# Kernel tuning notes

Hardware: AMD Instinct MI355X
Metric: run time of the kernel (lower is better)

## Reference

```python
import jax, jax.numpy as jnp
import numpy as np

DAMP_MIN = jnp.asarray([0.001, 0.001], dtype=jnp.float32)
B = 4194304


def setup_inputs() -> dict:
    key = jax.random.key(0)
    ks = jax.random.split(key, 14)
    rn = lambda k, s: jax.random.normal(k, s, dtype=jnp.float32)
    return {
        "x": rn(ks[0], (B, 2)),
        "w_d1": rn(ks[1], (2, 16)),
        "w_d2": rn(ks[2], (16, 16)),
        "w_d3": rn(ks[3], (16, 2)),
        "w_o1": rn(ks[4], (2, 16)),
        "w_o2": rn(ks[5], (16, 16)),
        "w_o3": rn(ks[6], (16, 1)),
        "b_d1": rn(ks[7], (16,)),
        "b_d2": rn(ks[8], (16,)),
        "b_d3": rn(ks[9], (2,)),
        "b_o1": rn(ks[10], (16,)),
        "b_o2": rn(ks[11], (16,)),
        "b_o3": rn(ks[12], (1,)),
    }


def reference(x, w_d1, w_d2, w_d3, w_o1, w_o2, w_o3,
              b_d1, b_d2, b_d3, b_o1, b_o2, b_o3) -> jnp.ndarray:
    # diag branch: 3-layer tanh MLP -> relu -> +damp_min -> * x   [B, 2]
    d = jnp.tanh(x @ w_d1 + b_d1)
    d = jnp.tanh(d @ w_d2 + b_d2)
    d3 = d @ w_d3 + b_d3
    d3r = (jax.nn.relu(d3) + DAMP_MIN) * x  # diag elements of L

    # off-diag branch: 3-layer tanh MLP -> scalar per sample   [B, 1]
    o = jnp.tanh(x @ w_o1 + b_o1)
    o = jnp.tanh(o @ w_o2 + b_o2)
    o3 = o @ w_o3 + b_o3

    # L = [[a, 0], [c, b]];  D_i = (L L^T) x_i, closed form for 2x2:
    # L L^T = [[a^2, a*c], [a*c, c^2 + b^2]]
    a = d3r[:, 0]
    b = d3r[:, 1]
    c = o3[:, 0]
    x0 = x[:, 0]
    x1 = x[:, 1]
    D0 = a * a * x0 + a * c * x1
    D1 = a * c * x0 + (c * c + b * b) * x1
    return jnp.stack([D0, D1], axis=1)  # [B, 2]
```

## Files before the change

### kernel.cpp

```cpp
#include <hip/hip_runtime.h>

#define BTOT 4194304
#define MPW 4

typedef __attribute__((ext_vector_type(4))) float f32x4;
typedef __attribute__((ext_vector_type(8))) short bf16x8;

__device__ __forceinline__ short f2bf(float f) {
  union { float f; unsigned u; } v; v.f = f;
  unsigned u = v.u;
  unsigned r = (u + 0x7FFFu + ((u >> 16) & 1u)) >> 16;
  return (short)r;
}
__device__ __forceinline__ float bf2f(short s) {
  union { unsigned u; float f; } v; v.u = ((unsigned)(unsigned short)s) << 16;
  return v.f;
}
__device__ __forceinline__ float tanh_fast(float x) {
  float t = __builtin_amdgcn_exp2f(x * 2.88539008177792681472f);
  float r = __builtin_amdgcn_rcpf(1.0f + t);
  return __builtin_fmaf(-2.0f, r, 1.0f);
}

__global__ __launch_bounds__(256, 4)
void damping_kernel(const float* __restrict__ x,
                    const float* __restrict__ w_d1, const float* __restrict__ w_d2,
                    const float* __restrict__ w_d3, const float* __restrict__ w_o1,
                    const float* __restrict__ w_o2, const float* __restrict__ w_o3,
                    const float* __restrict__ b_d1, const float* __restrict__ b_d2,
                    const float* __restrict__ b_d3, const float* __restrict__ b_o1,
                    const float* __restrict__ b_o2, const float* __restrict__ b_o3,
                    float* __restrict__ out)
{
  const int tid  = blockIdx.x * blockDim.x + threadIdx.x;
  const int wave = tid >> 6;
  const int l    = threadIdx.x & 63;
  const int g    = l >> 4;
  const int c16  = l & 15;
  const int kbase = g * 8;

  float W0[8], W1[8], B1[8];
  #pragma unroll
  for (int j = 0; j < 8; ++j) {
    int f = kbase + j;
    if (f < 16) { W0[j] = w_d1[f];      W1[j] = w_d1[16 + f];      B1[j] = b_d1[f]; }
    else        { W0[j] = w_o1[f - 16]; W1[j] = w_o1[16 + f - 16]; B1[j] = b_o1[f - 16]; }
  }
  bf16x8 Adh, Adl, Aoh, Aol;
  #pragma unroll
  for (int j = 0; j < 8; ++j) {
    int k = kbase + j;
    float ad = (k < 16)  ? w_d2[k * 16 + c16]        : 0.0f;
    float ao = (k >= 16) ? w_o2[(k - 16) * 16 + c16] : 0.0f;
    short adh = f2bf(ad); Adh[j] = adh; Adl[j] = f2bf(ad - bf2f(adh));
    short aoh = f2bf(ao); Aoh[j] = aoh; Aol[j] = f2bf(ao - bf2f(aoh));
  }
  f32x4 Cd0, Co0;
  float Wd30[4], Wd31[4], Wo3[4];
  #pragma unroll
  for (int i = 0; i < 4; ++i) {
    int f = g * 4 + i;
    Cd0[i] = b_d2[f]; Co0[i] = b_o2[f];
    Wd30[i] = w_d3[f * 2]; Wd31[i] = w_d3[f * 2 + 1]; Wo3[i] = w_o3[f];
  }
  const float bq0 = b_d3[0] * 0.25f, bq1 = b_d3[1] * 0.25f, bqo = b_o3[0] * 0.25f;

  for (int m = 0; m < MPW; ++m) {
    const int mbase = (wave * MPW + m) * 64;
    float o0 = 0.f, o1 = 0.f;
    #pragma unroll
    for (int t = 0; t < 4; ++t) {
      const int row = mbase + t * 16 + c16;
      const float2 xv = ((const float2*)x)[row];

      float h[8];
      #pragma unroll
      for (int j = 0; j < 8; ++j)
        h[j] = tanh_fast(__builtin_fmaf(xv.y, W1[j], __builtin_fmaf(xv.x, W0[j], B1[j])));

      bf16x8 bh, bl;
      #pragma unroll
      for (int j = 0; j < 8; ++j) {
        short hb = f2bf(h[j]); bh[j] = hb;
        bl[j] = f2bf(h[j] - bf2f(hb));
      }

      f32x4 accd = Cd0, acco = Co0;
      accd = __builtin_amdgcn_mfma_f32_16x16x32_bf16(Adh, bh, accd, 0, 0, 0);
      acco = __builtin_amdgcn_mfma_f32_16x16x32_bf16(Aoh, bh, acco, 0, 0, 0);
      accd = __builtin_amdgcn_mfma_f32_16x16x32_bf16(Adh, bl, accd, 0, 0, 0);
      acco = __builtin_amdgcn_mfma_f32_16x16x32_bf16(Aoh, bl, acco, 0, 0, 0);
      accd = __builtin_amdgcn_mfma_f32_16x16x32_bf16(Adl, bh, accd, 0, 0, 0);
      acco = __builtin_amdgcn_mfma_f32_16x16x32_bf16(Aol, bh, acco, 0, 0, 0);

      float pd0 = bq0, pd1 = bq1, po = bqo;
      #pragma unroll
      for (int i = 0; i < 4; ++i) {
        float dt = tanh_fast(accd[i]);
        float ot = tanh_fast(acco[i]);
        pd0 = __builtin_fmaf(dt, Wd30[i], pd0);
        pd1 = __builtin_fmaf(dt, Wd31[i], pd1);
        po  = __builtin_fmaf(ot, Wo3[i],  po);
      }
      pd0 += __shfl_xor(pd0, 16); pd0 += __shfl_xor(pd0, 32);
      pd1 += __shfl_xor(pd1, 16); pd1 += __shfl_xor(pd1, 32);
      po  += __shfl_xor(po, 16);  po  += __shfl_xor(po, 32);

      float a = (fmaxf(pd0, 0.f) + 0.001f) * xv.x;
      float b = (fmaxf(pd1, 0.f) + 0.001f) * xv.y;
      float c = po;
      float D0 = a * __builtin_fmaf(a, xv.x, c * xv.y);
      float s  = __builtin_fmaf(c, c, b * b);
      float D1 = __builtin_fmaf(a * c, xv.x, s * xv.y);

      if (t == g) { o0 = D0; o1 = D1; }
    }
    ((float2*)out)[mbase + l] = make_float2(o0, o1);
  }
}

extern "C" void kernel_launch(void* const* d_in, const int* in_sizes, int n_in,
                              void* d_out, int out_size, void* d_ws, size_t ws_size,
                              hipStream_t stream) {
  const float* x    = (const float*)d_in[0];
  const float* w_d1 = (const float*)d_in[1];
  const float* w_d2 = (const float*)d_in[2];
  const float* w_d3 = (const float*)d_in[3];
  const float* w_o1 = (const float*)d_in[4];
  const float* w_o2 = (const float*)d_in[5];
  const float* w_o3 = (const float*)d_in[6];
  const float* b_d1 = (const float*)d_in[7];
  const float* b_d2 = (const float*)d_in[8];
  const float* b_d3 = (const float*)d_in[9];
  const float* b_o1 = (const float*)d_in[10];
  const float* b_o2 = (const float*)d_in[11];
  const float* b_o3 = (const float*)d_in[12];
  float* out = (float*)d_out;

  const int waves  = BTOT / (64 * MPW);
  const int blocks = waves / 4;
  damping_kernel<<<blocks, 256, 0, stream>>>(x, w_d1, w_d2, w_d3, w_o1, w_o2, w_o3,
                                             b_d1, b_d2, b_d3, b_o1, b_o2, b_o3, out);
}
```

Baseline: 188.1 us.

## Fold tanh exp2 scaling into weights, cheapen hi/lo split, batch x loads

Pre-multiplies the first- and second-layer weights and biases by the exp2 scaling constant, so each tanh no longer needs its own multiply. The round-to-nearest bf16 hi/lo split of hidden activations becomes a truncating mask plus byte-permute packing, which takes fewer VALU ops. The four x loads per 64-row tile are also hoisted ahead of the compute loop to improve latency overlap. Truncation instead of rounding for the hi part slightly changes the split precision, but the lo term compensates for most of it.

```diff
diff --git a/kernel.cpp b/kernel.cpp
--- a/kernel.cpp
+++ b/kernel.cpp
@@ -5,6 +5,8 @@
 
 typedef __attribute__((ext_vector_type(4))) float f32x4;
 typedef __attribute__((ext_vector_type(8))) short bf16x8;
+
+#define KLOG 2.88539008177792681472f
 
 __device__ __forceinline__ short f2bf(float f) {
   union { float f; unsigned u; } v; v.f = f;
@@ -16,10 +18,29 @@
   union { unsigned u; float f; } v; v.u = ((unsigned)(unsigned short)s) << 16;
   return v.f;
 }
-__device__ __forceinline__ float tanh_fast(float x) {
-  float t = __builtin_amdgcn_exp2f(x * 2.88539008177792681472f);
+__device__ __forceinline__ float tanh_pre(float y) {
+  float t = __builtin_amdgcn_exp2f(y);
   float r = __builtin_amdgcn_rcpf(1.0f + t);
   return __builtin_fmaf(-2.0f, r, 1.0f);
+}
+
+__device__ __forceinline__ void pack_hilo(const float* h, bf16x8& bh, bf16x8& bl) {
+  union U { unsigned w[4]; bf16x8 v; } H, L;
+  #pragma unroll
+  for (int jw = 0; jw < 4; ++jw) {
+    float h0 = h[2 * jw], h1 = h[2 * jw + 1];
+    unsigned u0 = __builtin_bit_cast(unsigned, h0);
+    unsigned u1 = __builtin_bit_cast(unsigned, h1);
+    float hi0 = __builtin_bit_cast(float, u0 & 0xFFFF0000u);
+    float hi1 = __builtin_bit_cast(float, u1 & 0xFFFF0000u);
+    float lo0 = h0 - hi0;
+    float lo1 = h1 - hi1;
+    unsigned v0 = __builtin_bit_cast(unsigned, lo0);
+    unsigned v1 = __builtin_bit_cast(unsigned, lo1);
+    H.w[jw] = __builtin_amdgcn_perm(u1, u0, 0x07060302u);
+    L.w[jw] = __builtin_amdgcn_perm(v1, v0, 0x07060302u);
+  }
+  bh = H.v; bl = L.v;
 }
 
 __global__ __launch_bounds__(256, 4)
@@ -43,15 +64,15 @@
   #pragma unroll
   for (int j = 0; j < 8; ++j) {
     int f = kbase + j;
-    if (f < 16) { W0[j] = w_d1[f];      W1[j] = w_d1[16 + f];      B1[j] = b_d1[f]; }
-    else        { W0[j] = w_o1[f - 16]; W1[j] = w_o1[16 + f - 16]; B1[j] = b_o1[f - 16]; }
+    if (f < 16) { W0[j] = KLOG * w_d1[f];      W1[j] = KLOG * w_d1[16 + f];      B1[j] = KLOG * b_d1[f]; }
+    else        { W0[j] = KLOG * w_o1[f - 16]; W1[j] = KLOG * w_o1[16 + f - 16]; B1[j] = KLOG * b_o1[f - 16]; }
   }
   bf16x8 Adh, Adl, Aoh, Aol;
   #pragma unroll
   for (int j = 0; j < 8; ++j) {
     int k = kbase + j;
-    float ad = (k < 16)  ? w_d2[k * 16 + c16]        : 0.0f;
-    float ao = (k >= 16) ? w_o2[(k - 16) * 16 + c16] : 0.0f;
+    float ad = (k < 16)  ? KLOG * w_d2[k * 16 + c16]        : 0.0f;
+    float ao = (k >= 16) ? KLOG * w_o2[(k - 16) * 16 + c16] : 0.0f;
     short adh = f2bf(ad); Adh[j] = adh; Adl[j] = f2bf(ad - bf2f(adh));
     short aoh = f2bf(ao); Aoh[j] = aoh; Aol[j] = f2bf(ao - bf2f(aoh));
   }
@@ -60,30 +81,31 @@
   #pragma unroll
   for (int i = 0; i < 4; ++i) {
     int f = g * 4 + i;
-    Cd0[i] = b_d2[f]; Co0[i] = b_o2[f];
+    Cd0[i] = KLOG * b_d2[f]; Co0[i] = KLOG * b_o2[f];
     Wd30[i] = w_d3[f * 2]; Wd31[i] = w_d3[f * 2 + 1]; Wo3[i] = w_o3[f];
   }
   const float bq0 = b_d3[0] * 0.25f, bq1 = b_d3[1] * 0.25f, bqo = b_o3[0] * 0.25f;
 
   for (int m = 0; m < MPW; ++m) {
     const int mbase = (wave * MPW + m) * 64;
+
+    float2 xv4[4];
+    #pragma unroll
+    for (int t = 0; t < 4; ++t)
+      xv4[t] = ((const float2*)x)[mbase + t * 16 + c16];
+
     float o0 = 0.f, o1 = 0.f;
     #pragma unroll
     for (int t = 0; t < 4; ++t) {
-      const int row = mbase + t * 16 + c16;
-      const float2 xv = ((const float2*)x)[row];
+      const float2 xv = xv4[t];
 
       float h[8];
       #pragma unroll
       for (int j = 0; j < 8; ++j)
-        h[j] = tanh_fast(__builtin_fmaf(xv.y, W1[j], __builtin_fmaf(xv.x, W0[j], B1[j])));
+        h[j] = tanh_pre(__builtin_fmaf(xv.y, W1[j], __builtin_fmaf(xv.x, W0[j], B1[j])));
 
       bf16x8 bh, bl;
-      #pragma unroll
-      for (int j = 0; j < 8; ++j) {
-        short hb = f2bf(h[j]); bh[j] = hb;
-        bl[j] = f2bf(h[j] - bf2f(hb));
-      }
+      pack_hilo(h, bh, bl);
 
       f32x4 accd = Cd0, acco = Co0;
       accd = __builtin_amdgcn_mfma_f32_16x16x32_bf16(Adh, bh, accd, 0, 0, 0);
@@ -96,8 +118,8 @@
       float pd0 = bq0, pd1 = bq1, po = bqo;
       #pragma unroll
       for (int i = 0; i < 4; ++i) {
-        float dt = tanh_fast(accd[i]);
-        float ot = tanh_fast(acco[i]);
+        float dt = tanh_pre(accd[i]);
+        float ot = tanh_pre(acco[i]);
         pd0 = __builtin_fmaf(dt, Wd30[i], pd0);
         pd1 = __builtin_fmaf(dt, Wd31[i], pd1);
         po  = __builtin_fmaf(ot, Wo3[i],  po);
```

Result: faster. 174.4 us (-7.3%).
